# Performance work log

Measured on AMD Instinct MI355X. Metric: run time of the kernel, lower is better.

## Reference

```python
import jax, jax.numpy as jnp
import numpy as np
import math

N_PROP = 1000
NUM_CLASSES = 81
SCORE_THRESH = 0.05
NMS_THRESH = 0.5
DET_PER_IMG = 100
BBOX_XFORM_CLIP = math.log(1000.0 / 16.0)
WX, WY, WW, WH = 10.0, 10.0, 5.0, 5.0  # BoxCoder weights


def setup_inputs() -> dict:
    key = jax.random.key(0)
    k1, k2, k3, k4 = jax.random.split(key, 4)
    class_logits = jax.random.normal(k1, (N_PROP, NUM_CLASSES), dtype=jnp.float32) * 2.0
    box_regression = jax.random.normal(k2, (N_PROP, NUM_CLASSES * 4), dtype=jnp.float32) * 0.5
    # valid xyxy proposals inside an ~800x1333 image
    xy = jax.random.uniform(k3, (N_PROP, 2), dtype=jnp.float32) * jnp.array([1200.0, 700.0], jnp.float32)
    wh = jax.random.uniform(k4, (N_PROP, 2), dtype=jnp.float32) * 120.0 + 8.0
    concat_boxes = jnp.concatenate([xy, xy + wh], axis=1)
    return {"class_logits": class_logits, "box_regression": box_regression,
            "concat_boxes": concat_boxes, "image_height": 800, "image_width": 1333}


def decode(deltas, boxes):
    widths = boxes[:, 2] - boxes[:, 0] + 1.0
    heights = boxes[:, 3] - boxes[:, 1] + 1.0
    ctr_x = boxes[:, 0] + 0.5 * widths
    ctr_y = boxes[:, 1] + 0.5 * heights
    dx = deltas[:, 0::4] / WX
    dy = deltas[:, 1::4] / WY
    dw = jnp.minimum(deltas[:, 2::4] / WW, BBOX_XFORM_CLIP)
    dh = jnp.minimum(deltas[:, 3::4] / WH, BBOX_XFORM_CLIP)
    pred_ctr_x = dx * widths[:, None] + ctr_x[:, None]
    pred_ctr_y = dy * heights[:, None] + ctr_y[:, None]
    pred_w = jnp.exp(dw) * widths[:, None]
    pred_h = jnp.exp(dh) * heights[:, None]
    x1 = pred_ctr_x - 0.5 * pred_w
    y1 = pred_ctr_y - 0.5 * pred_h
    x2 = pred_ctr_x + 0.5 * pred_w - 1.0
    y2 = pred_ctr_y + 0.5 * pred_h - 1.0
    return jnp.stack([x1, y1, x2, y2], axis=-1)  # [N, C, 4]


def pairwise_iou(b):
    area = (b[:, 2] - b[:, 0] + 1.0) * (b[:, 3] - b[:, 1] + 1.0)  # [N]
    lt = jnp.maximum(b[:, None, :2], b[None, :, :2])
    rb = jnp.minimum(b[:, None, 2:], b[None, :, 2:])
    wh = jnp.clip(rb - lt + 1.0, 0.0)
    inter = wh[..., 0] * wh[..., 1]
    return inter / (area[:, None] + area[None, :] - inter)


def class_nms(boxes_c, scores_c):
    # boxes_c: [N,4], scores_c: [N] -> sorted scores/boxes and keep mask
    valid = scores_c > SCORE_THRESH
    order = jnp.argsort(-jnp.where(valid, scores_c, -jnp.inf))
    b = boxes_c[order]
    s = scores_c[order]
    v = valid[order]
    iou = pairwise_iou(b)  # [N, N]
    ar = jnp.arange(b.shape[0])

    def body(i, keep):
        sup = keep[i] & (iou[i] > NMS_THRESH) & (ar > i)
        return keep & (~sup)

    keep = jax.lax.fori_loop(0, b.shape[0], body, v)
    return s, b, keep


def reference(class_logits, box_regression, concat_boxes, image_height, image_width):
    probs = jax.nn.softmax(class_logits, axis=-1)          # [N, C]
    boxes_all = decode(box_regression, concat_boxes)        # [N, C, 4]
    # clip to image (clamp to [0, dim-1])
    w = jnp.float32(image_width)
    h = jnp.float32(image_height)
    clipped = jnp.stack([
        jnp.clip(boxes_all[..., 0], 0.0, w - 1.0),
        jnp.clip(boxes_all[..., 1], 0.0, h - 1.0),
        jnp.clip(boxes_all[..., 2], 0.0, w - 1.0),
        jnp.clip(boxes_all[..., 3], 0.0, h - 1.0),
    ], axis=-1)
    # skip background class 0; per-class NMS over foreground classes
    fg_boxes = jnp.transpose(clipped[:, 1:, :], (1, 0, 2))  # [C-1, N, 4]
    fg_scores = probs[:, 1:].T                               # [C-1, N]
    s, b, keep = jax.vmap(class_nms)(fg_boxes, fg_scores)
    cand = jnp.where(keep, s, -jnp.inf)                      # [C-1, N]
    flat_scores = cand.reshape(-1)
    flat_boxes = b.reshape(-1, 4)
    top_vals, top_idx = jax.lax.top_k(flat_scores, DET_PER_IMG)
    labels = (top_idx // N_PROP) + 1
    sel_boxes = flat_boxes[top_idx]
    valid = jnp.isfinite(top_vals)
    out_scores = jnp.where(valid, top_vals, 0.0)
    out_boxes = jnp.where(valid[:, None], sel_boxes, 0.0)
    out_labels = jnp.where(valid, labels, 0)
    return out_scores, out_boxes, out_labels
```

## Files before the change

### kernel.cpp

```cpp
#include <hip/hip_runtime.h>
#include <math.h>

#define N_PROP 1000
#define NUM_CLASSES 81
#define NFG 80
#define SCORE_THRESH 0.05f
#define NMS_THRESH 0.5f
#define DET_PER_IMG 100
#define PER_CLASS_CAP 100
#define KEPT_CAP (NFG * PER_CLASS_CAP)
#define MBITS 512
#define SURV_CAP 4800
#define BBOX_XFORM_CLIP 4.135166556742356f

__global__ __launch_bounds__(128) void k_decode(
    const float* __restrict__ logits,
    float* __restrict__ candS)
{
    const int n = blockIdx.x;
    const int t = threadIdx.x;
    __shared__ float redm[2];
    __shared__ float reds[2];

    float l = (t < NUM_CLASSES) ? logits[n * NUM_CLASSES + t] : -INFINITY;

    float m = l;
    #pragma unroll
    for (int o = 32; o > 0; o >>= 1) m = fmaxf(m, __shfl_xor(m, o));
    const int wave = t >> 6;
    if ((t & 63) == 0) redm[wave] = m;
    __syncthreads();
    m = fmaxf(redm[0], redm[1]);

    float e = (t < NUM_CLASSES) ? expf(l - m) : 0.0f;
    float s = e;
    #pragma unroll
    for (int o = 32; o > 0; o >>= 1) s += __shfl_xor(s, o);
    if ((t & 63) == 0) reds[wave] = s;
    __syncthreads();
    s = reds[0] + reds[1];

    if (t >= 1 && t < NUM_CLASSES) {
        const float prob = e / s;
        candS[(size_t)(t - 1) * N_PROP + n] = (prob > SCORE_THRESH) ? prob : 0.0f;
    }
}

__global__ __launch_bounds__(256) void k_nms(
    const float* __restrict__ candS,
    const float* __restrict__ deltas,
    const float* __restrict__ pboxes,
    const int* __restrict__ ih, const int* __restrict__ iw,
    float* __restrict__ keptScore,
    unsigned* __restrict__ keptKey,
    float4* __restrict__ keptBox)
{
    const int c   = blockIdx.x;
    const int cls = c + 1;
    const int tid = threadIdx.x;

    __shared__ union {
        struct { float ss[N_PROP]; int si[N_PROP]; float sb[N_PROP * 4]; } in;
        unsigned long long msk[MBITS * (MBITS / 64)];
    } u;
    __shared__ float os[N_PROP];
    __shared__ float ob[N_PROP * 4];
    __shared__ unsigned long long keepw_s[16];
    __shared__ int cnt;

    if (tid == 0) cnt = 0;
    __syncthreads();

    const float W = (float)iw[0] - 1.0f;
    const float H = (float)ih[0] - 1.0f;

    for (int n = tid; n < N_PROP; n += 256) {
        const float p = candS[(size_t)c * N_PROP + n];
        if (p > 0.0f) {
            const float x1b = pboxes[n * 4 + 0];
            const float y1b = pboxes[n * 4 + 1];
            const float x2b = pboxes[n * 4 + 2];
            const float y2b = pboxes[n * 4 + 3];
            const float w  = x2b - x1b + 1.0f;
            const float h  = y2b - y1b + 1.0f;
            const float cx = x1b + 0.5f * w;
            const float cy = y1b + 0.5f * h;
            const float* d = deltas + (size_t)n * (NUM_CLASSES * 4) + cls * 4;
            const float dx = d[0] / 10.0f;
            const float dy = d[1] / 10.0f;
            const float dw = fminf(d[2] / 5.0f, BBOX_XFORM_CLIP);
            const float dh = fminf(d[3] / 5.0f, BBOX_XFORM_CLIP);
            const float pcx = dx * w + cx;
            const float pcy = dy * h + cy;
            const float pw  = expf(dw) * w;
            const float ph  = expf(dh) * h;
            float X1 = pcx - 0.5f * pw;
            float Y1 = pcy - 0.5f * ph;
            float X2 = pcx + 0.5f * pw - 1.0f;
            float Y2 = pcy + 0.5f * ph - 1.0f;
            X1 = fminf(fmaxf(X1, 0.0f), W);
            Y1 = fminf(fmaxf(Y1, 0.0f), H);
            X2 = fminf(fmaxf(X2, 0.0f), W);
            Y2 = fminf(fmaxf(Y2, 0.0f), H);

            const int pos = atomicAdd(&cnt, 1);
            u.in.ss[pos] = p;
            u.in.si[pos] = n;
            u.in.sb[pos * 4 + 0] = X1;
            u.in.sb[pos * 4 + 1] = Y1;
            u.in.sb[pos * 4 + 2] = X2;
            u.in.sb[pos * 4 + 3] = Y2;
        }
    }
    __syncthreads();
    const int M = cnt;

    for (int i = tid; i < M; i += 256) {
        const float s0 = u.in.ss[i];
        const int   i0 = u.in.si[i];
        int r = 0;
        for (int j = 0; j < M; ++j) {
            const float sj = u.in.ss[j];
            r += (sj > s0) || (sj == s0 && u.in.si[j] < i0);
        }
        os[r] = s0;
        ob[r * 4 + 0] = u.in.sb[i * 4 + 0];
        ob[r * 4 + 1] = u.in.sb[i * 4 + 1];
        ob[r * 4 + 2] = u.in.sb[i * 4 + 2];
        ob[r * 4 + 3] = u.in.sb[i * 4 + 3];
    }
    __syncthreads();

    if (M <= MBITS) {
        const int NW = (M + 63) >> 6;

        for (int idx = tid; idx < M * NW; idx += 256) {
            const int i = idx / NW;
            const int w = idx - i * NW;
            const float ax1 = ob[i * 4 + 0], ay1 = ob[i * 4 + 1];
            const float ax2 = ob[i * 4 + 2], ay2 = ob[i * 4 + 3];
            const float aarea = (ax2 - ax1 + 1.0f) * (ay2 - ay1 + 1.0f);
            unsigned long long bits = 0;
            const int j0 = w << 6;
            const int jb = (i + 1 > j0) ? (i + 1) : j0;
            const int je = (j0 + 64 < M) ? (j0 + 64) : M;
            for (int j = jb; j < je; ++j) {
                const float bx1 = ob[j * 4 + 0], by1 = ob[j * 4 + 1];
                const float bx2 = ob[j * 4 + 2], by2 = ob[j * 4 + 3];
                const float barea = (bx2 - bx1 + 1.0f) * (by2 - by1 + 1.0f);
                const float ix1 = fmaxf(ax1, bx1), iy1 = fmaxf(ay1, by1);
                const float ix2 = fminf(ax2, bx2), iy2 = fminf(ay2, by2);
                const float iw_ = fmaxf(ix2 - ix1 + 1.0f, 0.0f);
                const float ih_ = fmaxf(iy2 - iy1 + 1.0f, 0.0f);
                const float inter = iw_ * ih_;
                const float iou = inter / (aarea + barea - inter);
                if (iou > NMS_THRESH) bits |= 1ull << (j - j0);
            }
            u.msk[i * NW + w] = bits;
        }
        __syncthreads();

        if (tid < 64) {
            const int l = tid;
            const int base = l << 6;
            int nb = M - base;
            nb = nb < 0 ? 0 : (nb > 64 ? 64 : nb);
            unsigned long long keepw =
                (nb == 64) ? ~0ull : ((nb == 0) ? 0ull : ((1ull << nb) - 1ull));
            for (int i = 0; i < M; ++i) {
                const unsigned long long kb = __shfl(keepw, i >> 6);
                if ((kb >> (i & 63)) & 1ull) {
                    const unsigned long long mrow =
                        (l < NW) ? u.msk[i * NW + l] : 0ull;
                    keepw &= ~mrow;
                }
            }
            if (l < 16) keepw_s[l] = keepw;
        }
        __syncthreads();

        unsigned long long kw[16];
        #pragma unroll
        for (int w = 0; w < 16; ++w) kw[w] = keepw_s[w];
        int S = 0;
        #pragma unroll
        for (int w = 0; w < 16; ++w) S += __popcll(kw[w]);
        if (S > PER_CLASS_CAP) S = PER_CLASS_CAP;

        for (int i = tid; i < M; i += 256) {
            const int w = i >> 6, b = i & 63;
            if ((kw[w] >> b) & 1ull) {
                int sr = 0;
                for (int ww = 0; ww < w; ++ww) sr += __popcll(kw[ww]);
                sr += __popcll(kw[w] & ((b == 0) ? 0ull : (~0ull >> (64 - b))));
                if (sr < PER_CLASS_CAP) {
                    const int slot = c * PER_CLASS_CAP + sr;
                    keptScore[slot] = os[i];
                    keptKey[slot]   = (unsigned)(c * N_PROP + i);
                    keptBox[slot]   = make_float4(ob[i * 4 + 0], ob[i * 4 + 1],
                                                  ob[i * 4 + 2], ob[i * 4 + 3]);
                }
            }
        }
        for (int s = S + tid; s < PER_CLASS_CAP; s += 256) {
            const int slot = c * PER_CLASS_CAP + s;
            keptScore[slot] = 0.0f;
            keptKey[slot]   = (unsigned)(c * N_PROP + s);
            keptBox[slot]   = make_float4(0.0f, 0.0f, 0.0f, 0.0f);
        }
    } else {
        int* ok = (int*)u.msk;
        for (int i = tid; i < M; i += 256) ok[i] = 1;
        __syncthreads();
        for (int i = 0; i < M; ++i) {
            if (ok[i]) {
                const float ax1 = ob[i * 4 + 0], ay1 = ob[i * 4 + 1];
                const float ax2 = ob[i * 4 + 2], ay2 = ob[i * 4 + 3];
                const float aarea = (ax2 - ax1 + 1.0f) * (ay2 - ay1 + 1.0f);
                for (int j = i + 1 + tid; j < M; j += 256) {
                    const float bx1 = ob[j * 4 + 0], by1 = ob[j * 4 + 1];
                    const float bx2 = ob[j * 4 + 2], by2 = ob[j * 4 + 3];
                    const float barea = (bx2 - bx1 + 1.0f) * (by2 - by1 + 1.0f);
                    const float ix1 = fmaxf(ax1, bx1), iy1 = fmaxf(ay1, by1);
                    const float ix2 = fminf(ax2, bx2), iy2 = fminf(ay2, by2);
                    const float iw_ = fmaxf(ix2 - ix1 + 1.0f, 0.0f);
                    const float ih_ = fmaxf(iy2 - iy1 + 1.0f, 0.0f);
                    const float inter = iw_ * ih_;
                    const float iou = inter / (aarea + barea - inter);
                    if (iou > NMS_THRESH) ok[j] = 0;
                }
            }
            __syncthreads();
        }
        for (int i = tid; i < M; i += 256) {
            if (ok[i]) {
                int sr = 0;
                for (int j = 0; j < i; ++j) sr += ok[j];
                if (sr < PER_CLASS_CAP) {
                    const int slot = c * PER_CLASS_CAP + sr;
                    keptScore[slot] = os[i];
                    keptKey[slot]   = (unsigned)(c * N_PROP + i);
                    keptBox[slot]   = make_float4(ob[i * 4 + 0], ob[i * 4 + 1],
                                                  ob[i * 4 + 2], ob[i * 4 + 3]);
                }
            }
        }
        int S = 0;
        for (int j = 0; j < M; ++j) S += ok[j];
        if (S > PER_CLASS_CAP) S = PER_CLASS_CAP;
        for (int s = S + tid; s < PER_CLASS_CAP; s += 256) {
            const int slot = c * PER_CLASS_CAP + s;
            keptScore[slot] = 0.0f;
            keptKey[slot]   = (unsigned)(c * N_PROP + s);
            keptBox[slot]   = make_float4(0.0f, 0.0f, 0.0f, 0.0f);
        }
    }
}

__device__ __forceinline__ int bucket_of_bits(unsigned bits) {
    int b = (int)(bits >> 16) - 15232;
    b = b < 0 ? 0 : b;
    return b > 1023 ? 1023 : b;
}

__global__ __launch_bounds__(1024) void k_topk(
    const float* __restrict__ keptScore,
    const unsigned* __restrict__ keptKey,
    const float4* __restrict__ keptBox,
    float* __restrict__ out)
{
    __shared__ union {
        struct {
            int hist[1024];
            int S[1024];
            unsigned long long spk[SURV_CAP];
            unsigned short sid[SURV_CAP];
        } sel;
        unsigned long long pk[KEPT_CAP];
    } u;
    __shared__ int ns_s;
    __shared__ int bstar_s;
    const int tid = threadIdx.x;

    u.sel.hist[tid] = 0;
    __syncthreads();

    for (int e = tid; e < KEPT_CAP; e += 1024) {
        const int b = bucket_of_bits(__float_as_uint(keptScore[e]));
        atomicAdd(&u.sel.hist[b], 1);
    }
    __syncthreads();

    u.sel.S[tid] = u.sel.hist[tid];
    __syncthreads();
    for (int d = 1; d < 1024; d <<= 1) {
        const int v = (tid + d < 1024) ? u.sel.S[tid + d] : 0;
        __syncthreads();
        u.sel.S[tid] += v;
        __syncthreads();
    }

    if (tid == 0) ns_s = 0;
    if (u.sel.S[tid] >= DET_PER_IMG &&
        (tid == 1023 || u.sel.S[tid + 1] < DET_PER_IMG))
        bstar_s = tid;
    __syncthreads();
    const int Bstar = bstar_s;

    for (int e = tid; e < KEPT_CAP; e += 1024) {
        const unsigned bits = __float_as_uint(keptScore[e]);
        if (bucket_of_bits(bits) >= Bstar) {
            const int pos = atomicAdd(&ns_s, 1);
            if (pos < SURV_CAP) {
                u.sel.spk[pos] = ((unsigned long long)bits << 32)
                               | (unsigned)(~keptKey[e]);
                u.sel.sid[pos] = (unsigned short)e;
            }
        }
    }
    __syncthreads();
    const int ns = ns_s;

    if (ns <= SURV_CAP) {
        for (int i = tid; i < ns; i += 1024) {
            const unsigned long long mykey = u.sel.spk[i];
            int r = 0;
            for (int j = 0; j < ns; ++j) r += (int)(u.sel.spk[j] > mykey);
            if (r < DET_PER_IMG) {
                const int e = u.sel.sid[i];
                const float sc = keptScore[e];
                const bool valid = sc > 0.0f;
                out[r] = sc;
                const float4 b = keptBox[e];
                out[DET_PER_IMG + r * 4 + 0] = b.x;
                out[DET_PER_IMG + r * 4 + 1] = b.y;
                out[DET_PER_IMG + r * 4 + 2] = b.z;
                out[DET_PER_IMG + r * 4 + 3] = b.w;
                const unsigned key = keptKey[e];
                out[DET_PER_IMG * 5 + r] = valid ? (float)(key / N_PROP + 1) : 0.0f;
            }
        }
    } else {
        __syncthreads();
        for (int j = tid; j < KEPT_CAP; j += 1024)
            u.pk[j] = ((unsigned long long)__float_as_uint(keptScore[j]) << 32)
                    | (unsigned)(~keptKey[j]);
        __syncthreads();
        for (int e = tid; e < KEPT_CAP; e += 1024) {
            const unsigned long long mykey = u.pk[e];
            int r = 0;
            for (int j = 0; j < KEPT_CAP; ++j) r += (int)(u.pk[j] > mykey);
            if (r < DET_PER_IMG) {
                const float sc = keptScore[e];
                const bool valid = sc > 0.0f;
                out[r] = sc;
                const float4 b = keptBox[e];
                out[DET_PER_IMG + r * 4 + 0] = b.x;
                out[DET_PER_IMG + r * 4 + 1] = b.y;
                out[DET_PER_IMG + r * 4 + 2] = b.z;
                out[DET_PER_IMG + r * 4 + 3] = b.w;
                const unsigned key = keptKey[e];
                out[DET_PER_IMG * 5 + r] = valid ? (float)(key / N_PROP + 1) : 0.0f;
            }
        }
    }
}

extern "C" void kernel_launch(void* const* d_in, const int* in_sizes, int n_in,
                              void* d_out, int out_size, void* d_ws, size_t ws_size,
                              hipStream_t stream) {
    const float* logits = (const float*)d_in[0];
    const float* deltas = (const float*)d_in[1];
    const float* pboxes = (const float*)d_in[2];
    const int*   ih     = (const int*)d_in[3];
    const int*   iw     = (const int*)d_in[4];
    float* out = (float*)d_out;

    char* p = (char*)d_ws;
    float4*   keptBox   = (float4*)p;    p += (size_t)KEPT_CAP * 16;
    float*    candS     = (float*)p;     p += (size_t)NFG * N_PROP * 4;
    float*    keptScore = (float*)p;     p += (size_t)KEPT_CAP * 4;
    unsigned* keptKey   = (unsigned*)p;  p += (size_t)KEPT_CAP * 4;

    k_decode<<<N_PROP, 128, 0, stream>>>(logits, candS);
    k_nms<<<NFG, 256, 0, stream>>>(candS, deltas, pboxes, ih, iw,
                                   keptScore, keptKey, keptBox);
    k_topk<<<1, 1024, 0, stream>>>(keptScore, keptKey, keptBox, out);
}
```

Before: 49.12 us.

## Fuse decode, per-class NMS and top-k into one persistent kernel with atomic barriers

The three launches (softmax/threshold, per-class NMS, global top-k) become a single 125-block, 1024-thread kernel. Each block first computes softmax for 8 proposals. Blocks then take a ticket from a global atomic counter: the last 80 blocks spin until all blocks finish phase one and each runs NMS for one class, and the last of those runs the top-k selection. The goal is to remove two kernel launch gaps. In exchange it adds a memset launch, spin-waits that assume all 125 blocks are co-resident, and moves NMS from 256 to 1024 threads per class, which leaves many threads idle in the serial parts.

```diff
diff --git a/kernel.cpp b/kernel.cpp
--- a/kernel.cpp
+++ b/kernel.cpp
@@ -11,70 +11,109 @@
 #define KEPT_CAP (NFG * PER_CLASS_CAP)
 #define MBITS 512
 #define SURV_CAP 4800
+#define NBLK 125
+#define WSTART (NBLK - NFG)
 #define BBOX_XFORM_CLIP 4.135166556742356f
 
-__global__ __launch_bounds__(128) void k_decode(
+__device__ __forceinline__ int bucket_of_bits(unsigned bits) {
+    int b = (int)(bits >> 16) - 15232;
+    b = b < 0 ? 0 : b;
+    return b > 1023 ? 1023 : b;
+}
+
+__global__ __launch_bounds__(1024, 1) void k_fused(
     const float* __restrict__ logits,
-    float* __restrict__ candS)
-{
-    const int n = blockIdx.x;
-    const int t = threadIdx.x;
-    __shared__ float redm[2];
-    __shared__ float reds[2];
-
-    float l = (t < NUM_CLASSES) ? logits[n * NUM_CLASSES + t] : -INFINITY;
-
-    float m = l;
-    #pragma unroll
-    for (int o = 32; o > 0; o >>= 1) m = fmaxf(m, __shfl_xor(m, o));
-    const int wave = t >> 6;
-    if ((t & 63) == 0) redm[wave] = m;
-    __syncthreads();
-    m = fmaxf(redm[0], redm[1]);
-
-    float e = (t < NUM_CLASSES) ? expf(l - m) : 0.0f;
-    float s = e;
-    #pragma unroll
-    for (int o = 32; o > 0; o >>= 1) s += __shfl_xor(s, o);
-    if ((t & 63) == 0) reds[wave] = s;
-    __syncthreads();
-    s = reds[0] + reds[1];
-
-    if (t >= 1 && t < NUM_CLASSES) {
-        const float prob = e / s;
-        candS[(size_t)(t - 1) * N_PROP + n] = (prob > SCORE_THRESH) ? prob : 0.0f;
-    }
-}
-
-__global__ __launch_bounds__(256) void k_nms(
-    const float* __restrict__ candS,
     const float* __restrict__ deltas,
     const float* __restrict__ pboxes,
     const int* __restrict__ ih, const int* __restrict__ iw,
+    int* __restrict__ done,
+    float* __restrict__ candS,
     float* __restrict__ keptScore,
     unsigned* __restrict__ keptKey,
-    float4* __restrict__ keptBox)
+    float4* __restrict__ keptBox,
+    float* __restrict__ out)
 {
-    const int c   = blockIdx.x;
+    const int tid = threadIdx.x;
+
+    __shared__ union {
+        struct {
+            union {
+                struct { float ss[N_PROP]; int si[N_PROP]; float sb[N_PROP * 4]; } in;
+                unsigned long long msk[MBITS * (MBITS / 64)];
+            } u;
+            float os[N_PROP];
+            float ob[N_PROP * 4];
+            unsigned long long keepw[16];
+        } p2;
+        struct {
+            int hist[1024];
+            int S[1024];
+            unsigned long long spk[SURV_CAP];
+            unsigned short sid[SURV_CAP];
+        } p3;
+        unsigned long long pk[KEPT_CAP];
+    } sm;
+    __shared__ float redm[8][2];
+    __shared__ float reds[8][2];
+    __shared__ int vsh;
+    __shared__ int cnt;
+    __shared__ int ns_s;
+    __shared__ int bstar_s;
+
+    {
+        const int sub = tid >> 7;
+        const int t   = tid & 127;
+        const int n   = blockIdx.x * 8 + sub;
+        const int wh  = t >> 6;
+
+        float l = (t < NUM_CLASSES) ? logits[n * NUM_CLASSES + t] : -INFINITY;
+
+        float m = l;
+        #pragma unroll
+        for (int o = 32; o > 0; o >>= 1) m = fmaxf(m, __shfl_xor(m, o));
+        if ((t & 63) == 0) redm[sub][wh] = m;
+        __syncthreads();
+        m = fmaxf(redm[sub][0], redm[sub][1]);
+
+        float e = (t < NUM_CLASSES) ? expf(l - m) : 0.0f;
+        float s = e;
+        #pragma unroll
+        for (int o = 32; o > 0; o >>= 1) s += __shfl_xor(s, o);
+        if ((t & 63) == 0) reds[sub][wh] = s;
+        __syncthreads();
+        s = reds[sub][0] + reds[sub][1];
+
+        if (t >= 1 && t < NUM_CLASSES) {
+            const float prob = e / s;
+            candS[(size_t)(t - 1) * N_PROP + n] = (prob > SCORE_THRESH) ? prob : 0.0f;
+        }
+    }
+
+    __threadfence();
+    __syncthreads();
+    if (tid == 0)
+        vsh = __hip_atomic_fetch_add(&done[0], 1, __ATOMIC_ACQ_REL,
+                                     __HIP_MEMORY_SCOPE_AGENT);
+    __syncthreads();
+    const int v = vsh;
+    if (v < WSTART) return;
+    const int c = v - WSTART;
+
+    if (tid == 0) {
+        while (__hip_atomic_load(&done[0], __ATOMIC_ACQUIRE,
+                                 __HIP_MEMORY_SCOPE_AGENT) < NBLK) {}
+    }
+    __syncthreads();
+    __threadfence();
+
     const int cls = c + 1;
-    const int tid = threadIdx.x;
-
-    __shared__ union {
-        struct { float ss[N_PROP]; int si[N_PROP]; float sb[N_PROP * 4]; } in;
-        unsigned long long msk[MBITS * (MBITS / 64)];
-    } u;
-    __shared__ float os[N_PROP];
-    __shared__ float ob[N_PROP * 4];
-    __shared__ unsigned long long keepw_s[16];
-    __shared__ int cnt;
-
     if (tid == 0) cnt = 0;
     __syncthreads();
 
     const float W = (float)iw[0] - 1.0f;
     const float H = (float)ih[0] - 1.0f;
 
-    for (int n = tid; n < N_PROP; n += 256) {
+    for (int n = tid; n < N_PROP; n += 1024) {
         const float p = candS[(size_t)c * N_PROP + n];
         if (p > 0.0f) {
             const float x1b = pboxes[n * 4 + 0];
@@ -104,49 +143,49 @@
             Y2 = fminf(fmaxf(Y2, 0.0f), H);
 
             const int pos = atomicAdd(&cnt, 1);
-            u.in.ss[pos] = p;
-            u.in.si[pos] = n;
-            u.in.sb[pos * 4 + 0] = X1;
-            u.in.sb[pos * 4 + 1] = Y1;
-            u.in.sb[pos * 4 + 2] = X2;
-            u.in.sb[pos * 4 + 3] = Y2;
+            sm.p2.u.in.ss[pos] = p;
+            sm.p2.u.in.si[pos] = n;
+            sm.p2.u.in.sb[pos * 4 + 0] = X1;
+            sm.p2.u.in.sb[pos * 4 + 1] = Y1;
+            sm.p2.u.in.sb[pos * 4 + 2] = X2;
+            sm.p2.u.in.sb[pos * 4 + 3] = Y2;
         }
     }
     __syncthreads();
     const int M = cnt;
 
-    for (int i = tid; i < M; i += 256) {
-        const float s0 = u.in.ss[i];
-        const int   i0 = u.in.si[i];
+    for (int i = tid; i < M; i += 1024) {
+        const float s0 = sm.p2.u.in.ss[i];
+        const int   i0 = sm.p2.u.in.si[i];
         int r = 0;
         for (int j = 0; j < M; ++j) {
-            const float sj = u.in.ss[j];
-            r += (sj > s0) || (sj == s0 && u.in.si[j] < i0);
-        }
-        os[r] = s0;
-        ob[r * 4 + 0] = u.in.sb[i * 4 + 0];
-        ob[r * 4 + 1] = u.in.sb[i * 4 + 1];
-        ob[r * 4 + 2] = u.in.sb[i * 4 + 2];
-        ob[r * 4 + 3] = u.in.sb[i * 4 + 3];
+            const float sj = sm.p2.u.in.ss[j];
+            r += (sj > s0) || (sj == s0 && sm.p2.u.in.si[j] < i0);
+        }
+        sm.p2.os[r] = s0;
+        sm.p2.ob[r * 4 + 0] = sm.p2.u.in.sb[i * 4 + 0];
+        sm.p2.ob[r * 4 + 1] = sm.p2.u.in.sb[i * 4 + 1];
+        sm.p2.ob[r * 4 + 2] = sm.p2.u.in.sb[i * 4 + 2];
+        sm.p2.ob[r * 4 + 3] = sm.p2.u.in.sb[i * 4 + 3];
     }
     __syncthreads();
 
     if (M <= MBITS) {
         const int NW = (M + 63) >> 6;
 
-        for (int idx = tid; idx < M * NW; idx += 256) {
+        for (int idx = tid; idx < M * NW; idx += 1024) {
             const int i = idx / NW;
             const int w = idx - i * NW;
-            const float ax1 = ob[i * 4 + 0], ay1 = ob[i * 4 + 1];
-            const float ax2 = ob[i * 4 + 2], ay2 = ob[i * 4 + 3];
+            const float ax1 = sm.p2.ob[i * 4 + 0], ay1 = sm.p2.ob[i * 4 + 1];
+            const float ax2 = sm.p2.ob[i * 4 + 2], ay2 = sm.p2.ob[i * 4 + 3];
             const float aarea = (ax2 - ax1 + 1.0f) * (ay2 - ay1 + 1.0f);
             unsigned long long bits = 0;
             const int j0 = w << 6;
             const int jb = (i + 1 > j0) ? (i + 1) : j0;
             const int je = (j0 + 64 < M) ? (j0 + 64) : M;
             for (int j = jb; j < je; ++j) {
-                const float bx1 = ob[j * 4 + 0], by1 = ob[j * 4 + 1];
-                const float bx2 = ob[j * 4 + 2], by2 = ob[j * 4 + 3];
+                const float bx1 = sm.p2.ob[j * 4 + 0], by1 = sm.p2.ob[j * 4 + 1];
+                const float bx2 = sm.p2.ob[j * 4 + 2], by2 = sm.p2.ob[j * 4 + 3];
                 const float barea = (bx2 - bx1 + 1.0f) * (by2 - by1 + 1.0f);
                 const float ix1 = fmaxf(ax1, bx1), iy1 = fmaxf(ay1, by1);
                 const float ix2 = fminf(ax2, bx2), iy2 = fminf(ay2, by2);
@@ -156,7 +195,7 @@
                 const float iou = inter / (aarea + barea - inter);
                 if (iou > NMS_THRESH) bits |= 1ull << (j - j0);
             }
-            u.msk[i * NW + w] = bits;
+            sm.p2.u.msk[i * NW + w] = bits;
         }
         __syncthreads();
 
@@ -171,23 +210,23 @@
                 const unsigned long long kb = __shfl(keepw, i >> 6);
                 if ((kb >> (i & 63)) & 1ull) {
                     const unsigned long long mrow =
-                        (l < NW) ? u.msk[i * NW + l] : 0ull;
+                        (l < NW) ? sm.p2.u.msk[i * NW + l] : 0ull;
                     keepw &= ~mrow;
                 }
             }
-            if (l < 16) keepw_s[l] = keepw;
+            if (l < 16) sm.p2.keepw[l] = keepw;
         }
         __syncthreads();
 
         unsigned long long kw[16];
         #pragma unroll
-        for (int w = 0; w < 16; ++w) kw[w] = keepw_s[w];
+        for (int w = 0; w < 16; ++w) kw[w] = sm.p2.keepw[w];
         int S = 0;
         #pragma unroll
         for (int w = 0; w < 16; ++w) S += __popcll(kw[w]);
         if (S > PER_CLASS_CAP) S = PER_CLASS_CAP;
 
-        for (int i = tid; i < M; i += 256) {
+        for (int i = tid; i < M; i += 1024) {
             const int w = i >> 6, b = i & 63;
             if ((kw[w] >> b) & 1ull) {
                 int sr = 0;
@@ -195,31 +234,31 @@
                 sr += __popcll(kw[w] & ((b == 0) ? 0ull : (~0ull >> (64 - b))));
                 if (sr < PER_CLASS_CAP) {
                     const int slot = c * PER_CLASS_CAP + sr;
-                    keptScore[slot] = os[i];
+                    keptScore[slot] = sm.p2.os[i];
                     keptKey[slot]   = (unsigned)(c * N_PROP + i);
-                    keptBox[slot]   = make_float4(ob[i * 4 + 0], ob[i * 4 + 1],
-                                                  ob[i * 4 + 2], ob[i * 4 + 3]);
+                    keptBox[slot]   = make_float4(sm.p2.ob[i * 4 + 0], sm.p2.ob[i * 4 + 1],
+                                                  sm.p2.ob[i * 4 + 2], sm.p2.ob[i * 4 + 3]);
                 }
             }
         }
-        for (int s = S + tid; s < PER_CLASS_CAP; s += 256) {
+        for (int s = S + tid; s < PER_CLASS_CAP; s += 1024) {
             const int slot = c * PER_CLASS_CAP + s;
             keptScore[slot] = 0.0f;
             keptKey[slot]   = (unsigned)(c * N_PROP + s);
             keptBox[slot]   = make_float4(0.0f, 0.0f, 0.0f, 0.0f);
         }
     } else {
-        int* ok = (int*)u.msk;
-        for (int i = tid; i < M; i += 256) ok[i] = 1;
+        int* ok = (int*)sm.p2.u.msk;
+        for (int i = tid; i < M; i += 1024) ok[i] = 1;
         __syncthreads();
         for (int i = 0; i < M; ++i) {
             if (ok[i]) {
-                const float ax1 = ob[i * 4 + 0], ay1 = ob[i * 4 + 1];
-                const float ax2 = ob[i * 4 + 2], ay2 = ob[i * 4 + 3];
+                const float ax1 = sm.p2.ob[i * 4 + 0], ay1 = sm.p2.ob[i * 4 + 1];
+                const float ax2 = sm.p2.ob[i * 4 + 2], ay2 = sm.p2.ob[i * 4 + 3];
                 const float aarea = (ax2 - ax1 + 1.0f) * (ay2 - ay1 + 1.0f);
-                for (int j = i + 1 + tid; j < M; j += 256) {
-                    const float bx1 = ob[j * 4 + 0], by1 = ob[j * 4 + 1];
-                    const float bx2 = ob[j * 4 + 2], by2 = ob[j * 4 + 3];
+                for (int j = i + 1 + tid; j < M; j += 1024) {
+                    const float bx1 = sm.p2.ob[j * 4 + 0], by1 = sm.p2.ob[j * 4 + 1];
+                    const float bx2 = sm.p2.ob[j * 4 + 2], by2 = sm.p2.ob[j * 4 + 3];
                     const float barea = (bx2 - bx1 + 1.0f) * (by2 - by1 + 1.0f);
                     const float ix1 = fmaxf(ax1, bx1), iy1 = fmaxf(ay1, by1);
                     const float ix2 = fminf(ax2, bx2), iy2 = fminf(ay2, by2);
@@ -232,77 +271,61 @@
             }
             __syncthreads();
         }
-        for (int i = tid; i < M; i += 256) {
+        for (int i = tid; i < M; i += 1024) {
             if (ok[i]) {
                 int sr = 0;
                 for (int j = 0; j < i; ++j) sr += ok[j];
                 if (sr < PER_CLASS_CAP) {
                     const int slot = c * PER_CLASS_CAP + sr;
-                    keptScore[slot] = os[i];
+                    keptScore[slot] = sm.p2.os[i];
                     keptKey[slot]   = (unsigned)(c * N_PROP + i);
-                    keptBox[slot]   = make_float4(ob[i * 4 + 0], ob[i * 4 + 1],
-                                                  ob[i * 4 + 2], ob[i * 4 + 3]);
+                    keptBox[slot]   = make_float4(sm.p2.ob[i * 4 + 0], sm.p2.ob[i * 4 + 1],
+                                                  sm.p2.ob[i * 4 + 2], sm.p2.ob[i * 4 + 3]);
                 }
             }
         }
         int S = 0;
         for (int j = 0; j < M; ++j) S += ok[j];
         if (S > PER_CLASS_CAP) S = PER_CLASS_CAP;
-        for (int s = S + tid; s < PER_CLASS_CAP; s += 256) {
+        for (int s = S + tid; s < PER_CLASS_CAP; s += 1024) {
             const int slot = c * PER_CLASS_CAP + s;
             keptScore[slot] = 0.0f;
             keptKey[slot]   = (unsigned)(c * N_PROP + s);
             keptBox[slot]   = make_float4(0.0f, 0.0f, 0.0f, 0.0f);
         }
     }
-}
-
-__device__ __forceinline__ int bucket_of_bits(unsigned bits) {
-    int b = (int)(bits >> 16) - 15232;
-    b = b < 0 ? 0 : b;
-    return b > 1023 ? 1023 : b;
-}
-
-__global__ __launch_bounds__(1024) void k_topk(
-    const float* __restrict__ keptScore,
-    const unsigned* __restrict__ keptKey,
-    const float4* __restrict__ keptBox,
-    float* __restrict__ out)
-{
-    __shared__ union {
-        struct {
-            int hist[1024];
-            int S[1024];
-            unsigned long long spk[SURV_CAP];
-            unsigned short sid[SURV_CAP];
-        } sel;
-        unsigned long long pk[KEPT_CAP];
-    } u;
-    __shared__ int ns_s;
-    __shared__ int bstar_s;
-    const int tid = threadIdx.x;
-
-    u.sel.hist[tid] = 0;
+
+    __threadfence();
+    __syncthreads();
+    if (tid == 0)
+        vsh = __hip_atomic_fetch_add(&done[1], 1, __ATOMIC_ACQ_REL,
+                                     __HIP_MEMORY_SCOPE_AGENT);
+    __syncthreads();
+    if (vsh != NFG - 1) return;
+    __threadfence();
+    __syncthreads();
+
+    sm.p3.hist[tid] = 0;
     __syncthreads();
 
     for (int e = tid; e < KEPT_CAP; e += 1024) {
         const int b = bucket_of_bits(__float_as_uint(keptScore[e]));
-        atomicAdd(&u.sel.hist[b], 1);
-    }
-    __syncthreads();
-
-    u.sel.S[tid] = u.sel.hist[tid];
+        atomicAdd(&sm.p3.hist[b], 1);
+    }
+    __syncthreads();
+
+    sm.p3.S[tid] = sm.p3.hist[tid];
     __syncthreads();
     for (int d = 1; d < 1024; d <<= 1) {
-        const int v = (tid + d < 1024) ? u.sel.S[tid + d] : 0;
-        __syncthreads();
-        u.sel.S[tid] += v;
+        const int x = (tid + d < 1024) ? sm.p3.S[tid + d] : 0;
+        __syncthreads();
+        sm.p3.S[tid] += x;
         __syncthreads();
     }
 
     if (tid == 0) ns_s = 0;
-    if (u.sel.S[tid] >= DET_PER_IMG &&
-        (tid == 1023 || u.sel.S[tid + 1] < DET_PER_IMG))
+    if (sm.p3.S[tid] >= DET_PER_IMG &&
+        (tid == 1023 || sm.p3.S[tid + 1] < DET_PER_IMG))
         bstar_s = tid;
     __syncthreads();
     const int Bstar = bstar_s;
@@ -312,9 +335,9 @@
         if (bucket_of_bits(bits) >= Bstar) {
             const int pos = atomicAdd(&ns_s, 1);
             if (pos < SURV_CAP) {
-                u.sel.spk[pos] = ((unsigned long long)bits << 32)
+                sm.p3.spk[pos] = ((unsigned long long)bits << 32)
                                | (unsigned)(~keptKey[e]);
-                u.sel.sid[pos] = (unsigned short)e;
+                sm.p3.sid[pos] = (unsigned short)e;
             }
         }
     }
@@ -323,11 +346,11 @@
 
     if (ns <= SURV_CAP) {
         for (int i = tid; i < ns; i += 1024) {
-            const unsigned long long mykey = u.sel.spk[i];
+            const unsigned long long mykey = sm.p3.spk[i];
             int r = 0;
-            for (int j = 0; j < ns; ++j) r += (int)(u.sel.spk[j] > mykey);
+            for (int j = 0; j < ns; ++j) r += (int)(sm.p3.spk[j] > mykey);
             if (r < DET_PER_IMG) {
-                const int e = u.sel.sid[i];
+                const int e = sm.p3.sid[i];
                 const float sc = keptScore[e];
                 const bool valid = sc > 0.0f;
                 out[r] = sc;
@@ -343,13 +366,13 @@
     } else {
         __syncthreads();
         for (int j = tid; j < KEPT_CAP; j += 1024)
-            u.pk[j] = ((unsigned long long)__float_as_uint(keptScore[j]) << 32)
-                    | (unsigned)(~keptKey[j]);
+            sm.pk[j] = ((unsigned long long)__float_as_uint(keptScore[j]) << 32)
+                     | (unsigned)(~keptKey[j]);
         __syncthreads();
         for (int e = tid; e < KEPT_CAP; e += 1024) {
-            const unsigned long long mykey = u.pk[e];
+            const unsigned long long mykey = sm.pk[e];
             int r = 0;
-            for (int j = 0; j < KEPT_CAP; ++j) r += (int)(u.pk[j] > mykey);
+            for (int j = 0; j < KEPT_CAP; ++j) r += (int)(sm.pk[j] > mykey);
             if (r < DET_PER_IMG) {
                 const float sc = keptScore[e];
                 const bool valid = sc > 0.0f;
@@ -376,14 +399,14 @@
     const int*   iw     = (const int*)d_in[4];
     float* out = (float*)d_out;
 
-    char* p = (char*)d_ws;
+    int* done = (int*)d_ws;
+    char* p = (char*)d_ws + 256;
     float4*   keptBox   = (float4*)p;    p += (size_t)KEPT_CAP * 16;
     float*    candS     = (float*)p;     p += (size_t)NFG * N_PROP * 4;
     float*    keptScore = (float*)p;     p += (size_t)KEPT_CAP * 4;
     unsigned* keptKey   = (unsigned*)p;  p += (size_t)KEPT_CAP * 4;
 
-    k_decode<<<N_PROP, 128, 0, stream>>>(logits, candS);
-    k_nms<<<NFG, 256, 0, stream>>>(candS, deltas, pboxes, ih, iw,
-                                   keptScore, keptKey, keptBox);
-    k_topk<<<1, 1024, 0, stream>>>(keptScore, keptKey, keptBox, out);
+    hipMemsetAsync(done, 0, 16, stream);
+    k_fused<<<NBLK, 1024, 0, stream>>>(logits, deltas, pboxes, ih, iw,
+                                       done, candS, keptScore, keptKey, keptBox, out);
 }
```

Result: slower. 161.2 us (+228.1%).

## Fuse softmax into per-class NMS kernel and widen blocks to 1024 threads

Applied to the files above, without the earlier changes.

Removes the separate softmax kernel and its candS scratch buffer. Each NMS block now recomputes the full softmax row for every proposal, one thread per proposal, and keeps only its own class's probability. This saves a kernel launch and a global round trip. In exchange the softmax work is repeated 80 times, with strided per-thread row reads that do not coalesce, and the block grows to 1024 threads so every loop stride changes.

```diff
diff --git a/kernel.cpp b/kernel.cpp
--- a/kernel.cpp
+++ b/kernel.cpp
@@ -13,41 +13,8 @@
 #define SURV_CAP 4800
 #define BBOX_XFORM_CLIP 4.135166556742356f
 
-__global__ __launch_bounds__(128) void k_decode(
+__global__ __launch_bounds__(1024, 1) void k_nms(
     const float* __restrict__ logits,
-    float* __restrict__ candS)
-{
-    const int n = blockIdx.x;
-    const int t = threadIdx.x;
-    __shared__ float redm[2];
-    __shared__ float reds[2];
-
-    float l = (t < NUM_CLASSES) ? logits[n * NUM_CLASSES + t] : -INFINITY;
-
-    float m = l;
-    #pragma unroll
-    for (int o = 32; o > 0; o >>= 1) m = fmaxf(m, __shfl_xor(m, o));
-    const int wave = t >> 6;
-    if ((t & 63) == 0) redm[wave] = m;
-    __syncthreads();
-    m = fmaxf(redm[0], redm[1]);
-
-    float e = (t < NUM_CLASSES) ? expf(l - m) : 0.0f;
-    float s = e;
-    #pragma unroll
-    for (int o = 32; o > 0; o >>= 1) s += __shfl_xor(s, o);
-    if ((t & 63) == 0) reds[wave] = s;
-    __syncthreads();
-    s = reds[0] + reds[1];
-
-    if (t >= 1 && t < NUM_CLASSES) {
-        const float prob = e / s;
-        candS[(size_t)(t - 1) * N_PROP + n] = (prob > SCORE_THRESH) ? prob : 0.0f;
-    }
-}
-
-__global__ __launch_bounds__(256) void k_nms(
-    const float* __restrict__ candS,
     const float* __restrict__ deltas,
     const float* __restrict__ pboxes,
     const int* __restrict__ ih, const int* __restrict__ iw,
@@ -74,9 +41,18 @@
     const float W = (float)iw[0] - 1.0f;
     const float H = (float)ih[0] - 1.0f;
 
-    for (int n = tid; n < N_PROP; n += 256) {
-        const float p = candS[(size_t)c * N_PROP + n];
-        if (p > 0.0f) {
+    if (tid < N_PROP) {
+        const int n = tid;
+        const float* row = logits + (size_t)n * NUM_CLASSES;
+        float m = row[0];
+        #pragma unroll 8
+        for (int k = 1; k < NUM_CLASSES; ++k) m = fmaxf(m, row[k]);
+        float s = 0.0f;
+        #pragma unroll 8
+        for (int k = 0; k < NUM_CLASSES; ++k) s += expf(row[k] - m);
+        const float p = expf(row[cls] - m) / s;
+
+        if (p > SCORE_THRESH) {
             const float x1b = pboxes[n * 4 + 0];
             const float y1b = pboxes[n * 4 + 1];
             const float x2b = pboxes[n * 4 + 2];
@@ -115,7 +91,7 @@
     __syncthreads();
     const int M = cnt;
 
-    for (int i = tid; i < M; i += 256) {
+    for (int i = tid; i < M; i += 1024) {
         const float s0 = u.in.ss[i];
         const int   i0 = u.in.si[i];
         int r = 0;
@@ -134,7 +110,7 @@
     if (M <= MBITS) {
         const int NW = (M + 63) >> 6;
 
-        for (int idx = tid; idx < M * NW; idx += 256) {
+        for (int idx = tid; idx < M * NW; idx += 1024) {
             const int i = idx / NW;
             const int w = idx - i * NW;
             const float ax1 = ob[i * 4 + 0], ay1 = ob[i * 4 + 1];
@@ -187,7 +163,7 @@
         for (int w = 0; w < 16; ++w) S += __popcll(kw[w]);
         if (S > PER_CLASS_CAP) S = PER_CLASS_CAP;
 
-        for (int i = tid; i < M; i += 256) {
+        for (int i = tid; i < M; i += 1024) {
             const int w = i >> 6, b = i & 63;
             if ((kw[w] >> b) & 1ull) {
                 int sr = 0;
@@ -202,7 +178,7 @@
                 }
             }
         }
-        for (int s = S + tid; s < PER_CLASS_CAP; s += 256) {
+        for (int s = S + tid; s < PER_CLASS_CAP; s += 1024) {
             const int slot = c * PER_CLASS_CAP + s;
             keptScore[slot] = 0.0f;
             keptKey[slot]   = (unsigned)(c * N_PROP + s);
@@ -210,14 +186,14 @@
         }
     } else {
         int* ok = (int*)u.msk;
-        for (int i = tid; i < M; i += 256) ok[i] = 1;
+        for (int i = tid; i < M; i += 1024) ok[i] = 1;
         __syncthreads();
         for (int i = 0; i < M; ++i) {
             if (ok[i]) {
                 const float ax1 = ob[i * 4 + 0], ay1 = ob[i * 4 + 1];
                 const float ax2 = ob[i * 4 + 2], ay2 = ob[i * 4 + 3];
                 const float aarea = (ax2 - ax1 + 1.0f) * (ay2 - ay1 + 1.0f);
-                for (int j = i + 1 + tid; j < M; j += 256) {
+                for (int j = i + 1 + tid; j < M; j += 1024) {
                     const float bx1 = ob[j * 4 + 0], by1 = ob[j * 4 + 1];
                     const float bx2 = ob[j * 4 + 2], by2 = ob[j * 4 + 3];
                     const float barea = (bx2 - bx1 + 1.0f) * (by2 - by1 + 1.0f);
@@ -232,7 +208,7 @@
             }
             __syncthreads();
         }
-        for (int i = tid; i < M; i += 256) {
+        for (int i = tid; i < M; i += 1024) {
             if (ok[i]) {
                 int sr = 0;
                 for (int j = 0; j < i; ++j) sr += ok[j];
@@ -248,7 +224,7 @@
         int S = 0;
         for (int j = 0; j < M; ++j) S += ok[j];
         if (S > PER_CLASS_CAP) S = PER_CLASS_CAP;
-        for (int s = S + tid; s < PER_CLASS_CAP; s += 256) {
+        for (int s = S + tid; s < PER_CLASS_CAP; s += 1024) {
             const int slot = c * PER_CLASS_CAP + s;
             keptScore[slot] = 0.0f;
             keptKey[slot]   = (unsigned)(c * N_PROP + s);
@@ -378,12 +354,10 @@
 
     char* p = (char*)d_ws;
     float4*   keptBox   = (float4*)p;    p += (size_t)KEPT_CAP * 16;
-    float*    candS     = (float*)p;     p += (size_t)NFG * N_PROP * 4;
     float*    keptScore = (float*)p;     p += (size_t)KEPT_CAP * 4;
     unsigned* keptKey   = (unsigned*)p;  p += (size_t)KEPT_CAP * 4;
 
-    k_decode<<<N_PROP, 128, 0, stream>>>(logits, candS);
-    k_nms<<<NFG, 256, 0, stream>>>(candS, deltas, pboxes, ih, iw,
-                                   keptScore, keptKey, keptBox);
+    k_nms<<<NFG, 1024, 0, stream>>>(logits, deltas, pboxes, ih, iw,
+                                    keptScore, keptKey, keptBox);
     k_topk<<<1, 1024, 0, stream>>>(keptScore, keptKey, keptBox, out);
 }
```

New measurement: 73.12 us. 1.49x slower.
